# Optimization experiments

Hardware: AMD Instinct MI355X
Metric: run time of the kernel (lower is better)

## Reference

```python
import jax, jax.numpy as jnp
import numpy as np

N_NODES = 100000
N_EDGES = 800000
N_IN = 256
N_H = 128


def setup_inputs() -> dict:
    key = jax.random.key(0)
    ks = jax.random.split(key, 8)
    x_1 = jax.random.normal(ks[0], (1, N_NODES, N_IN), dtype=jnp.float32)
    x_2 = jax.random.normal(ks[1], (1, N_NODES, N_IN), dtype=jnp.float32)
    edge_index = jax.random.randint(ks[2], (2, N_EDGES), 0, N_NODES, dtype=jnp.int32)
    edge_weight = jax.random.uniform(ks[3], (N_EDGES,), dtype=jnp.float32)
    # xavier-uniform-ish init for fc weight (stored as [in, out])
    lim = float(np.sqrt(6.0 / (N_IN + N_H)))
    W_gcn = jax.random.uniform(ks[4], (N_IN, N_H), minval=-lim, maxval=lim, dtype=jnp.float32)
    gcn_bias = jnp.zeros((N_H,), dtype=jnp.float32)
    prelu_a = jnp.full((1,), 0.25, dtype=jnp.float32)  # PReLU default slope
    lim2 = float(np.sqrt(1.0 / N_H))
    lin_W = jax.random.uniform(ks[5], (N_H, N_H), minval=-lim2, maxval=lim2, dtype=jnp.float32)
    lin_b = jax.random.uniform(ks[6], (N_H,), minval=-lim2, maxval=lim2, dtype=jnp.float32)
    return {
        "x_1": x_1, "x_2": x_2, "edge_index": edge_index, "edge_weight": edge_weight,
        "W_gcn": W_gcn, "gcn_bias": gcn_bias, "prelu_a": prelu_a,
        "lin_W": lin_W, "lin_b": lin_b,
    }


def _prelu(x, a):
    return jnp.where(x >= 0, x, a * x)


def _gcn(feat, edge_index, edge_weight, W, b, a, n_nodes):
    # feat: [1, N, n_in] -> h: [N, n_h]
    h = jnp.squeeze(feat, 0) @ W
    row, col = edge_index[0], edge_index[1]
    # spmm: out[i] = sum_{e: row_e = i} w_e * h[col_e]
    msg = edge_weight[:, None] * h[col]            # [E, n_h]
    agg = jax.ops.segment_sum(msg, row, num_segments=n_nodes)  # [N, n_h]
    return _prelu(agg + b, a)                      # [N, n_h]


def reference(x_1, x_2, edge_index, edge_weight, W_gcn, gcn_bias, prelu_a, lin_W, lin_b):
    n = x_1.shape[1]
    h_1 = _gcn(x_1, edge_index, edge_weight, W_gcn, gcn_bias, prelu_a, n)
    h_2 = _gcn(x_2, edge_index, edge_weight, W_gcn, gcn_bias, prelu_a, n)
    z_1 = (h_1 @ lin_W + lin_b).sum(1)   # [N]
    z_2 = (h_2 @ lin_W + lin_b).sum(1)   # [N]
    return jnp.concatenate((z_1, z_2), 0)  # [2N]
```

## Files before the change

### kernel.cpp

```cpp
#include <hip/hip_runtime.h>

#define N_NODES 100000
#define N_EDGES 800000
#define N_IN    256
#define N_H     128
#define M_TOT   (2 * N_NODES)

typedef __bf16 bfx8 __attribute__((ext_vector_type(8)));
typedef unsigned short u16x8 __attribute__((ext_vector_type(8)));
typedef float fx4 __attribute__((ext_vector_type(4)));

__device__ inline unsigned short f2bf(float f) {
    union { float f; unsigned u; } v; v.f = f;
    return (unsigned short)((v.u + 0x7FFF + ((v.u >> 16) & 1)) >> 16);
}
__device__ inline float bf2f(unsigned short s) {
    union { unsigned u; float f; } v; v.u = ((unsigned)s) << 16;
    return v.f;
}

#define WT_S 264

__global__ __launch_bounds__(256, 2) void gemm_kernel(
        const float* __restrict__ x1, const float* __restrict__ x2,
        const unsigned short* __restrict__ wT,
        unsigned short* __restrict__ hb) {
    __shared__ unsigned short wl[N_H * WT_S];
    const int t = threadIdx.x;
#pragma unroll
    for (int i = 0; i < 16; ++i) {
        int f  = t + i * 256;
        int n  = f >> 5;
        int kp = (f & 31) * 8;
        *(u16x8*)(wl + n * WT_S + kp) = *(const u16x8*)(wT + n * N_IN + kp);
    }
    __syncthreads();

    const int wave = t >> 6, lane = t & 63;
    const int quad = lane >> 4, l16 = lane & 15;
    const int mw = blockIdx.x * 64 + wave * 16;
    const float* x = (mw < N_NODES) ? x1 : x2;
    const int mrow = (mw < N_NODES) ? mw : mw - N_NODES;

    fx4 acc[8];
#pragma unroll
    for (int c = 0; c < 8; ++c) acc[c] = (fx4){0.f, 0.f, 0.f, 0.f};

    const float* xrow = x + (size_t)(mrow + l16) * N_IN;
#pragma unroll
    for (int kk = 0; kk < N_IN; kk += 32) {
        float4 a0 = *(const float4*)(xrow + kk + quad * 8);
        float4 a1 = *(const float4*)(xrow + kk + quad * 8 + 4);
        u16x8 au;
        au[0] = f2bf(a0.x); au[1] = f2bf(a0.y); au[2] = f2bf(a0.z); au[3] = f2bf(a0.w);
        au[4] = f2bf(a1.x); au[5] = f2bf(a1.y); au[6] = f2bf(a1.z); au[7] = f2bf(a1.w);
        bfx8 af = __builtin_bit_cast(bfx8, au);
#pragma unroll
        for (int c = 0; c < 8; ++c) {
            bfx8 bf = *(const bfx8*)(wl + (size_t)(c * 16 + l16) * WT_S + kk + quad * 8);
            acc[c] = __builtin_amdgcn_mfma_f32_16x16x32_bf16(af, bf, acc[c], 0, 0, 0);
        }
    }
#pragma unroll
    for (int c = 0; c < 8; ++c)
#pragma unroll
        for (int r = 0; r < 4; ++r)
            hb[(size_t)(mw + quad * 4 + r) * N_H + c * 16 + l16] = f2bf(acc[c][r]);
}

__global__ __launch_bounds__(256) void hist_kernel(const int* __restrict__ ei,
                                                   int* __restrict__ deg) {
    int e = blockIdx.x * 256 + threadIdx.x;
    if (e < N_EDGES) atomicAdd(deg + ei[e], 1);
}

__global__ __launch_bounds__(256) void scan1_kernel(const int* __restrict__ deg,
                                                    int* __restrict__ part,
                                                    int* __restrict__ bsum) {
    __shared__ int s[256];
    int g = blockIdx.x * 256 + threadIdx.x;
    int v = (g < N_NODES) ? deg[g] : 0;
    s[threadIdx.x] = v;
    __syncthreads();
#pragma unroll
    for (int off = 1; off < 256; off <<= 1) {
        int t = (threadIdx.x >= off) ? s[threadIdx.x - off] : 0;
        __syncthreads();
        s[threadIdx.x] += t;
        __syncthreads();
    }
    if (g < N_NODES) part[g] = s[threadIdx.x] - v;
    if (threadIdx.x == 255) bsum[blockIdx.x] = s[255];
}

#define NBLK_SCAN 391
__global__ void scan2_kernel(int* __restrict__ bsum) {
    __shared__ int s[512];
    int v = (threadIdx.x < NBLK_SCAN) ? bsum[threadIdx.x] : 0;
    s[threadIdx.x] = v;
    __syncthreads();
#pragma unroll
    for (int off = 1; off < 512; off <<= 1) {
        int t = (threadIdx.x >= off) ? s[threadIdx.x - off] : 0;
        __syncthreads();
        s[threadIdx.x] += t;
        __syncthreads();
    }
    if (threadIdx.x < NBLK_SCAN) bsum[threadIdx.x] = s[threadIdx.x] - v;
}

__global__ __launch_bounds__(256) void scan3_kernel(const int* __restrict__ part,
                                                    const int* __restrict__ bsum,
                                                    int* __restrict__ off,
                                                    int* __restrict__ cursor) {
    int g = blockIdx.x * 256 + threadIdx.x;
    if (g < N_NODES) {
        int o = part[g] + bsum[blockIdx.x];
        off[g] = o;
        cursor[g] = o;
    }
    if (g == 0) off[N_NODES] = N_EDGES;
}

__global__ __launch_bounds__(256) void scatter_kernel(const int* __restrict__ ei,
                                                      const float* __restrict__ ew,
                                                      int* __restrict__ cursor,
                                                      int2* __restrict__ edata) {
    int e = blockIdx.x * 256 + threadIdx.x;
    if (e >= N_EDGES) return;
    int row = ei[e];
    int pos = atomicAdd(cursor + row, 1);
    edata[pos] = make_int2(ei[N_EDGES + e], __float_as_int(ew[e]));
}

__global__ __launch_bounds__(256) void gcn_seg_kernel(const int* __restrict__ off,
                                                      const int2* __restrict__ edata,
                                                      const unsigned short* __restrict__ hb,
                                                      const float* __restrict__ gcn_bias,
                                                      const float* __restrict__ prelu_a,
                                                      const float* __restrict__ wsum,
                                                      float* __restrict__ zout) {
    const int wave = threadIdx.x >> 6, lane = threadIdx.x & 63;
    const int node = blockIdx.x * 4 + wave;
    const unsigned short* h = hb;
    float* z = zout;
    int n = node;
    if (node >= N_NODES) { h += (size_t)N_NODES * N_H; z += N_NODES; n -= N_NODES; }
    const int s = off[n], e = off[n + 1];
    float a0 = 0.f, a1 = 0.f;
    int i = s;
    for (; i + 1 < e; i += 2) {
        int2 e0 = edata[i], e1 = edata[i + 1];
        float w0 = __int_as_float(e0.y), w1 = __int_as_float(e1.y);
        ushort2 h0 = *(const ushort2*)(h + (size_t)e0.x * N_H + lane * 2);
        ushort2 h1 = *(const ushort2*)(h + (size_t)e1.x * N_H + lane * 2);
        a0 += w0 * bf2f(h0.x) + w1 * bf2f(h1.x);
        a1 += w0 * bf2f(h0.y) + w1 * bf2f(h1.y);
    }
    if (i < e) {
        int2 e0 = edata[i];
        float w0 = __int_as_float(e0.y);
        ushort2 h0 = *(const ushort2*)(h + (size_t)e0.x * N_H + lane * 2);
        a0 += w0 * bf2f(h0.x);
        a1 += w0 * bf2f(h0.y);
    }
    const float alpha = prelu_a[0];
    float v0 = a0 + gcn_bias[2 * lane];
    float v1 = a1 + gcn_bias[2 * lane + 1];
    v0 = (v0 >= 0.f) ? v0 : alpha * v0;
    v1 = (v1 >= 0.f) ? v1 : alpha * v1;
    float sres = v0 * wsum[2 * lane] + v1 * wsum[2 * lane + 1];
#pragma unroll
    for (int o = 32; o; o >>= 1) sres += __shfl_down(sres, o, 64);
    if (lane == 0) z[n] = sres + wsum[128];
}

__global__ void wprep_kernel(const float* __restrict__ W,
                             const float* __restrict__ linW,
                             const float* __restrict__ linb,
                             unsigned short* __restrict__ wT,
                             float* __restrict__ wsum) {
    if (blockIdx.x == 0) {
        int t = threadIdx.x;
        for (int i = 0; i < (N_IN * N_H) / 256; ++i) {
            int o = i * 256 + t;
            int n = o >> 8, k = o & 255;
            wT[o] = f2bf(W[(size_t)k * N_H + n]);
        }
    } else {
        int j = threadIdx.x;
        if (j < N_H) {
            float s = 0.f;
            for (int o = 0; o < N_H; ++o) s += linW[j * N_H + o];
            wsum[j] = s;
        }
        if (j == N_H) {
            float s = 0.f;
            for (int o = 0; o < N_H; ++o) s += linb[o];
            wsum[N_H] = s;
        }
    }
}

extern "C" void kernel_launch(void* const* d_in, const int* in_sizes, int n_in,
                              void* d_out, int out_size, void* d_ws, size_t ws_size,
                              hipStream_t stream) {
    const float* x1 = (const float*)d_in[0];
    const float* x2 = (const float*)d_in[1];
    const int*   ei = (const int*)d_in[2];
    const float* ew = (const float*)d_in[3];
    const float* Wg = (const float*)d_in[4];
    const float* gb = (const float*)d_in[5];
    const float* pa = (const float*)d_in[6];
    const float* lW = (const float*)d_in[7];
    const float* lb = (const float*)d_in[8];
    float* zout = (float*)d_out;

    unsigned short* hb   = (unsigned short*)d_ws;
    int2*  edata  = (int2*)(hb + (size_t)M_TOT * N_H);
    unsigned short* wT   = (unsigned short*)(edata + N_EDGES);
    int*   deg    = (int*)(wT + N_IN * N_H);
    int*   part   = deg + 100096;
    int*   off    = part + 100096;
    int*   cursor = off + 100096;
    int*   bsum   = cursor + 100096;
    float* wsum   = (float*)(bsum + 512);

    wprep_kernel<<<2, 256, 0, stream>>>(Wg, lW, lb, wT, wsum);

    hipMemsetAsync(deg, 0, (size_t)N_NODES * sizeof(int), stream);
    hist_kernel<<<(N_EDGES + 255) / 256, 256, 0, stream>>>(ei, deg);
    scan1_kernel<<<NBLK_SCAN, 256, 0, stream>>>(deg, part, bsum);
    scan2_kernel<<<1, 512, 0, stream>>>(bsum);
    scan3_kernel<<<NBLK_SCAN, 256, 0, stream>>>(part, bsum, off, cursor);
    scatter_kernel<<<(N_EDGES + 255) / 256, 256, 0, stream>>>(ei, ew, cursor, edata);

    gemm_kernel<<<M_TOT / 64, 256, 0, stream>>>(x1, x2, wT, hb);
    gcn_seg_kernel<<<M_TOT / 4, 256, 0, stream>>>(off, edata, hb, gb, pa, wsum, zout);
}
```

Measured before the change: 467.2 us.

## Fuse GEMM with edge scatter, merge prep kernels, aggregate both views per edge list

Merges the weight-prep and degree-histogram kernels into one launch and parallelises the W transpose across 32 blocks. The GEMM now runs 512-thread blocks in the same grid as the CSR edge scatter, so the two can overlap. The aggregation kernel processes both graph views per node, reading each edge entry once and gathering from both h halves, with the column pre-multiplied by N_H and the offsets made wave-uniform. This halves edge-list traffic and cuts launch count, at the cost of larger LDS/thread blocks and mixed work in one grid.

```diff
diff --git a/kernel.cpp b/kernel.cpp
--- a/kernel.cpp
+++ b/kernel.cpp
@@ -20,16 +20,29 @@
 }
 
 #define WT_S 264
-
-__global__ __launch_bounds__(256, 2) void gemm_kernel(
+#define NGB  1563
+#define NSB  1563
+
+__global__ __launch_bounds__(512, 2) void gemm_scatter_kernel(
         const float* __restrict__ x1, const float* __restrict__ x2,
         const unsigned short* __restrict__ wT,
-        unsigned short* __restrict__ hb) {
+        unsigned short* __restrict__ hb,
+        const int* __restrict__ ei, const float* __restrict__ ew,
+        int* __restrict__ cursor, int2* __restrict__ edata) {
+    const int t = threadIdx.x;
+    if (blockIdx.x >= NGB) {
+        int e = (blockIdx.x - NGB) * 512 + t;
+        if (e < N_EDGES) {
+            int row = ei[e];
+            int pos = atomicAdd(cursor + row, 1);
+            edata[pos] = make_int2(ei[N_EDGES + e] * N_H, __float_as_int(ew[e]));
+        }
+        return;
+    }
     __shared__ unsigned short wl[N_H * WT_S];
-    const int t = threadIdx.x;
-#pragma unroll
-    for (int i = 0; i < 16; ++i) {
-        int f  = t + i * 256;
+#pragma unroll
+    for (int i = 0; i < 8; ++i) {
+        int f  = t + i * 512;
         int n  = f >> 5;
         int kp = (f & 31) * 8;
         *(u16x8*)(wl + n * WT_S + kp) = *(const u16x8*)(wT + n * N_IN + kp);
@@ -38,7 +51,8 @@
 
     const int wave = t >> 6, lane = t & 63;
     const int quad = lane >> 4, l16 = lane & 15;
-    const int mw = blockIdx.x * 64 + wave * 16;
+    const int mw = blockIdx.x * 128 + wave * 16;
+    if (mw >= M_TOT) return;
     const float* x = (mw < N_NODES) ? x1 : x2;
     const int mrow = (mw < N_NODES) ? mw : mw - N_NODES;
 
@@ -68,10 +82,39 @@
             hb[(size_t)(mw + quad * 4 + r) * N_H + c * 16 + l16] = f2bf(acc[c][r]);
 }
 
-__global__ __launch_bounds__(256) void hist_kernel(const int* __restrict__ ei,
-                                                   int* __restrict__ deg) {
-    int e = blockIdx.x * 256 + threadIdx.x;
-    if (e < N_EDGES) atomicAdd(deg + ei[e], 1);
+#define HIST_BLKS 3125
+__global__ __launch_bounds__(256) void prep_kernel(const int* __restrict__ ei,
+                                                   int* __restrict__ deg,
+                                                   const float* __restrict__ W,
+                                                   unsigned short* __restrict__ wT,
+                                                   const float* __restrict__ linW,
+                                                   const float* __restrict__ linb,
+                                                   float* __restrict__ wsum) {
+    const int t = threadIdx.x;
+    if (blockIdx.x < HIST_BLKS) {
+        int e = blockIdx.x * 256 + t;
+        if (e < N_EDGES) atomicAdd(deg + ei[e], 1);
+    } else if (blockIdx.x < HIST_BLKS + 32) {
+        int kb = (blockIdx.x - HIST_BLKS) * 8;
+#pragma unroll
+        for (int p = 0; p < 4; ++p) {
+            int idx = p * 256 + t;
+            int k = kb + (idx >> 7), n = idx & 127;
+            wT[(size_t)n * N_IN + k] = f2bf(W[(size_t)k * N_H + n]);
+        }
+    } else {
+        int j = t;
+        if (j < N_H) {
+            float s = 0.f;
+            for (int o = 0; o < N_H; ++o) s += linW[j * N_H + o];
+            wsum[j] = s;
+        }
+        if (j == N_H) {
+            float s = 0.f;
+            for (int o = 0; o < N_H; ++o) s += linb[o];
+            wsum[N_H] = s;
+        }
+    }
 }
 
 __global__ __launch_bounds__(256) void scan1_kernel(const int* __restrict__ deg,
@@ -122,17 +165,6 @@
     if (g == 0) off[N_NODES] = N_EDGES;
 }
 
-__global__ __launch_bounds__(256) void scatter_kernel(const int* __restrict__ ei,
-                                                      const float* __restrict__ ew,
-                                                      int* __restrict__ cursor,
-                                                      int2* __restrict__ edata) {
-    int e = blockIdx.x * 256 + threadIdx.x;
-    if (e >= N_EDGES) return;
-    int row = ei[e];
-    int pos = atomicAdd(cursor + row, 1);
-    edata[pos] = make_int2(ei[N_EDGES + e], __float_as_int(ew[e]));
-}
-
 __global__ __launch_bounds__(256) void gcn_seg_kernel(const int* __restrict__ off,
                                                       const int2* __restrict__ edata,
                                                       const unsigned short* __restrict__ hb,
@@ -142,63 +174,55 @@
                                                       float* __restrict__ zout) {
     const int wave = threadIdx.x >> 6, lane = threadIdx.x & 63;
     const int node = blockIdx.x * 4 + wave;
-    const unsigned short* h = hb;
-    float* z = zout;
-    int n = node;
-    if (node >= N_NODES) { h += (size_t)N_NODES * N_H; z += N_NODES; n -= N_NODES; }
-    const int s = off[n], e = off[n + 1];
+    const unsigned short* h1 = hb;
+    const unsigned short* h2 = hb + (size_t)N_NODES * N_H;
+    const int s = __builtin_amdgcn_readfirstlane(off[node]);
+    const int e = __builtin_amdgcn_readfirstlane(off[node + 1]);
+    const int l2 = lane * 2;
     float a0 = 0.f, a1 = 0.f;
+    float b0 = 0.f, b1 = 0.f;
     int i = s;
     for (; i + 1 < e; i += 2) {
-        int2 e0 = edata[i], e1 = edata[i + 1];
-        float w0 = __int_as_float(e0.y), w1 = __int_as_float(e1.y);
-        ushort2 h0 = *(const ushort2*)(h + (size_t)e0.x * N_H + lane * 2);
-        ushort2 h1 = *(const ushort2*)(h + (size_t)e1.x * N_H + lane * 2);
-        a0 += w0 * bf2f(h0.x) + w1 * bf2f(h1.x);
-        a1 += w0 * bf2f(h0.y) + w1 * bf2f(h1.y);
+        int2 E0 = edata[i], E1 = edata[i + 1];
+        float w0 = __int_as_float(E0.y), w1 = __int_as_float(E1.y);
+        ushort2 p10 = *(const ushort2*)(h1 + E0.x + l2);
+        ushort2 p20 = *(const ushort2*)(h2 + E0.x + l2);
+        ushort2 p11 = *(const ushort2*)(h1 + E1.x + l2);
+        ushort2 p21 = *(const ushort2*)(h2 + E1.x + l2);
+        a0 += w0 * bf2f(p10.x) + w1 * bf2f(p11.x);
+        a1 += w0 * bf2f(p10.y) + w1 * bf2f(p11.y);
+        b0 += w0 * bf2f(p20.x) + w1 * bf2f(p21.x);
+        b1 += w0 * bf2f(p20.y) + w1 * bf2f(p21.y);
     }
     if (i < e) {
-        int2 e0 = edata[i];
-        float w0 = __int_as_float(e0.y);
-        ushort2 h0 = *(const ushort2*)(h + (size_t)e0.x * N_H + lane * 2);
-        a0 += w0 * bf2f(h0.x);
-        a1 += w0 * bf2f(h0.y);
+        int2 E0 = edata[i];
+        float w0 = __int_as_float(E0.y);
+        ushort2 p10 = *(const ushort2*)(h1 + E0.x + l2);
+        ushort2 p20 = *(const ushort2*)(h2 + E0.x + l2);
+        a0 += w0 * bf2f(p10.x);
+        a1 += w0 * bf2f(p10.y);
+        b0 += w0 * bf2f(p20.x);
+        b1 += w0 * bf2f(p20.y);
     }
     const float alpha = prelu_a[0];
-    float v0 = a0 + gcn_bias[2 * lane];
-    float v1 = a1 + gcn_bias[2 * lane + 1];
+    const float g0 = gcn_bias[l2], g1 = gcn_bias[l2 + 1];
+    const float q0 = wsum[l2],     q1 = wsum[l2 + 1];
+    float v0 = a0 + g0, v1 = a1 + g1;
+    float u0 = b0 + g0, u1 = b1 + g1;
     v0 = (v0 >= 0.f) ? v0 : alpha * v0;
     v1 = (v1 >= 0.f) ? v1 : alpha * v1;
-    float sres = v0 * wsum[2 * lane] + v1 * wsum[2 * lane + 1];
-#pragma unroll
-    for (int o = 32; o; o >>= 1) sres += __shfl_down(sres, o, 64);
-    if (lane == 0) z[n] = sres + wsum[128];
-}
-
-__global__ void wprep_kernel(const float* __restrict__ W,
-                             const float* __restrict__ linW,
-                             const float* __restrict__ linb,
-                             unsigned short* __restrict__ wT,
-                             float* __restrict__ wsum) {
-    if (blockIdx.x == 0) {
-        int t = threadIdx.x;
-        for (int i = 0; i < (N_IN * N_H) / 256; ++i) {
-            int o = i * 256 + t;
-            int n = o >> 8, k = o & 255;
-            wT[o] = f2bf(W[(size_t)k * N_H + n]);
-        }
-    } else {
-        int j = threadIdx.x;
-        if (j < N_H) {
-            float s = 0.f;
-            for (int o = 0; o < N_H; ++o) s += linW[j * N_H + o];
-            wsum[j] = s;
-        }
-        if (j == N_H) {
-            float s = 0.f;
-            for (int o = 0; o < N_H; ++o) s += linb[o];
-            wsum[N_H] = s;
-        }
+    u0 = (u0 >= 0.f) ? u0 : alpha * u0;
+    u1 = (u1 >= 0.f) ? u1 : alpha * u1;
+    float s1 = v0 * q0 + v1 * q1;
+    float s2 = u0 * q0 + u1 * q1;
+#pragma unroll
+    for (int o = 32; o; o >>= 1) {
+        s1 += __shfl_down(s1, o, 64);
+        s2 += __shfl_down(s2, o, 64);
+    }
+    if (lane == 0) {
+        zout[node]           = s1 + wsum[128];
+        zout[node + N_NODES] = s2 + wsum[128];
     }
 }
 
@@ -226,15 +250,12 @@
     int*   bsum   = cursor + 100096;
     float* wsum   = (float*)(bsum + 512);
 
-    wprep_kernel<<<2, 256, 0, stream>>>(Wg, lW, lb, wT, wsum);
-
     hipMemsetAsync(deg, 0, (size_t)N_NODES * sizeof(int), stream);
-    hist_kernel<<<(N_EDGES + 255) / 256, 256, 0, stream>>>(ei, deg);
+    prep_kernel<<<HIST_BLKS + 33, 256, 0, stream>>>(ei, deg, Wg, wT, lW, lb, wsum);
     scan1_kernel<<<NBLK_SCAN, 256, 0, stream>>>(deg, part, bsum);
     scan2_kernel<<<1, 512, 0, stream>>>(bsum);
     scan3_kernel<<<NBLK_SCAN, 256, 0, stream>>>(part, bsum, off, cursor);
-    scatter_kernel<<<(N_EDGES + 255) / 256, 256, 0, stream>>>(ei, ew, cursor, edata);
-
-    gemm_kernel<<<M_TOT / 64, 256, 0, stream>>>(x1, x2, wT, hb);
-    gcn_seg_kernel<<<M_TOT / 4, 256, 0, stream>>>(off, edata, hb, gb, pa, wsum, zout);
-}
+    gemm_scatter_kernel<<<NGB + NSB, 512, 0, stream>>>(x1, x2, wT, hb,
+                                                       ei, ew, cursor, edata);
+    gcn_seg_kernel<<<N_NODES / 4, 256, 0, stream>>>(off, edata, hb, gb, pa, wsum, zout);
+}
```

After: 392.3 us. 16.0% less time.
